# Performance work log

Hardware: AMD Instinct MI355X
Metric: run time of the kernel (lower is better)

Reference implementation:

```python
import jax, jax.numpy as jnp
import numpy as np

# static config (matches init_kwargs)
T_K = 3      # Time_kernel
K = 3        # spatial_kernel_side_length
C = 64       # dim_hidden
H = 4        # num_head
D = 16       # dim_head
NL = 2       # num_layers
F = 3        # dim_feature
N, S1, S2 = 32, 32, 32
P = K // 2
L1 = T_K // 2
M = T_K * K * K
EPS = 1e-5


def _neighbor_mask():
    # spatial_neighbor_mask with an all-ones city mask: offset (k1,k2) is a valid
    # neighbor of cell (s1,s2) iff it lands inside the grid.
    m = np.zeros((S1, S2, K, K), dtype=bool)
    s1 = np.arange(S1); s2 = np.arange(S2)
    for k1 in range(K):
        v1 = (s1 + k1 - P >= 0) & (s1 + k1 - P < S1)
        for k2 in range(K):
            v2 = (s2 + k2 - P >= 0) & (s2 + k2 - P < S2)
            m[:, :, k1, k2] = v1[:, None] & v2[None, :]
    mf = m.reshape(S1, S2, K * K)
    # tiled across Time_kernel, flattened in (t, k1, k2) order like the torch code
    return np.tile(mf[:, :, None, :], (1, 1, T_K, 1)).reshape(S1, S2, M)

_MASK = jnp.asarray(_neighbor_mask())


def _forward(x, W_in, b_in, W_out, b_out, Wq, bq, Wk, bk, Wv, bv):
    # BatchNorm2d (training-mode batch stats, affine = identity init)
    mean = x.mean(axis=(0, 1, 2))
    var = ((x - mean) ** 2).mean(axis=(0, 1, 2))
    h = (x - mean) * jax.lax.rsqrt(var + EPS)
    h = h @ W_in + b_in  # [N,S1,S2,C]

    for l in range(NL):
        res = h  # res_block_thickness = 1 -> residual every layer
        q = (h @ Wq[l] + bq[l]).reshape(N, S1, S2, H, D)
        # spatial unfold (nn.Unfold, padding=K//2, stride=1)
        hp = jnp.pad(h, ((0, 0), (P, P), (P, P), (0, 0)))
        u = jnp.stack([jnp.stack([hp[:, k1:k1 + S1, k2:k2 + S2, :]
                                  for k2 in range(K)]) for k1 in range(K)])  # [K,K,N,S1,S2,C]
        # time unfold (zero-padded shifts along N)
        up = jnp.pad(u, ((0, 0), (0, 0), (L1, L1), (0, 0), (0, 0), (0, 0)))
        ut = jnp.stack([up[:, :, t:t + N] for t in range(T_K)])  # [T,K,K,N,S1,S2,C]
        # per-offset single-Linear MLPs (kernel_neurons=[C,C]), batched over T,K,K
        ks = jnp.einsum('tijnabc,tijcd->nabtijd', ut, Wk[l]) + bk[l]
        vs = jnp.einsum('tijnabc,tijcd->nabtijd', ut, Wv[l]) + bv[l]
        kM = ks.reshape(N, S1, S2, M, H, D)
        vM = vs.reshape(N, S1, S2, M, H, D)
        # unscaled dot-product attention over valid neighbors (masked == dropped)
        sc = jnp.einsum('nabmhd,nabhd->nabhm', kM, q)
        sc = jnp.where(_MASK[None, :, :, None, :], sc, -1e30)
        w = jax.nn.softmax(sc, axis=-1)
        h = jnp.einsum('nabhm,nabmhd->nabhd', w, vM).reshape(N, S1, S2, C)
        h = h + res

    return h @ W_out + b_out  # [N,S1,S2,F]


def setup_inputs() -> dict:
    key = jax.random.key(0)
    k = jax.random.split(key, 11)
    s = 0.05
    return {
        'x': jax.random.normal(k[0], (N, S1, S2, F), jnp.float32),
        'W_in': jax.random.normal(k[1], (F, C), jnp.float32) * s,
        'b_in': jax.random.normal(k[2], (C,), jnp.float32) * s,
        'W_out': jax.random.normal(k[3], (C, F), jnp.float32) * s,
        'b_out': jax.random.normal(k[4], (F,), jnp.float32) * s,
        'Wq': jax.random.normal(k[5], (NL, C, C), jnp.float32) * s,
        'bq': jax.random.normal(k[6], (NL, C), jnp.float32) * s,
        'Wk': jax.random.normal(k[7], (NL, T_K, K, K, C, C), jnp.float32) * s,
        'bk': jax.random.normal(k[8], (NL, T_K, K, K, C), jnp.float32) * s,
        'Wv': jax.random.normal(k[9], (NL, T_K, K, K, C, C), jnp.float32) * s,
        'bv': jax.random.normal(k[10], (NL, T_K, K, K, C), jnp.float32) * s,
    }


def reference(x, W_in, b_in, W_out, b_out, Wq, bq, Wk, bk, Wv, bv):
    return _forward(x, W_in, b_in, W_out, b_out, Wq, bq, Wk, bk, Wv, bv)
```

## Files before the change

### kernel.cpp

```cpp
#include <hip/hip_runtime.h>
#include <hip/hip_bf16.h>


typedef short short8_t __attribute__((ext_vector_type(8)));
typedef float floatx16 __attribute__((ext_vector_type(16)));

__device__ __forceinline__ short f2bs(float f) {
    __hip_bfloat16 h = __float2bfloat16(f);
    return *reinterpret_cast<short*>(&h);
}
__device__ __forceinline__ float bs2f(short s) {
    union { unsigned u; float f; } v;
    v.u = ((unsigned)(unsigned short)s) << 16;
    return v.f;
}
__device__ __forceinline__ int hn_idx(int rowid, int chunk) {
    return rowid * 64 + ((chunk ^ (rowid & 7)) << 3);
}
__device__ __forceinline__ float half_sum(float p) {
    float a = p, b = p;
    asm("v_permlane32_swap_b32 %0, %1" : "+v"(a), "+v"(b));
    return a + b;
}

__global__ void prep_kernel(const float* __restrict__ Wq, const float* __restrict__ Wk,
                            const float* __restrict__ Wv, short* __restrict__ dst,
                            const float* __restrict__ x, float* __restrict__ sums) {
    if (blockIdx.x < 220) {
        int t = blockIdx.x * 256 + threadIdx.x;
        if (t >= 110 * 512) return;
        int mat  = t >> 9;
        int rem  = t & 511;
        int hp   = rem >> 8;
        int kk   = (rem >> 6) & 3;
        int lane = rem & 63;
        int krow = kk * 16 + ((lane >> 5) << 3);
        int col  = hp * 32 + (lane & 31);
        const float* W;
        if (mat < 2)       W = Wq + mat * 4096;
        else if (mat < 56) W = Wk + (mat - 2) * 4096;
        else               W = Wv + (mat - 56) * 4096;
        short8_t v;
        #pragma unroll
        for (int j = 0; j < 8; ++j) v[j] = f2bs(W[(krow + j) * 64 + col]);
        *(short8_t*)&dst[(size_t)mat * 4096 + ((hp * 4 + kk) * 64 + lane) * 8] = v;
    } else {
        int bid = blockIdx.x - 220;
        int t = bid * 256 + threadIdx.x;
        const float4* x4 = (const float4*)x;
        float4 v0 = x4[t * 3 + 0], v1 = x4[t * 3 + 1], v2 = x4[t * 3 + 2];
        float vv[6];
        vv[0] = v0.x + v0.w + v1.z + v2.y;
        vv[1] = v0.y + v1.x + v1.w + v2.z;
        vv[2] = v0.z + v1.y + v2.x + v2.w;
        vv[3] = v0.x*v0.x + v0.w*v0.w + v1.z*v1.z + v2.y*v2.y;
        vv[4] = v0.y*v0.y + v1.x*v1.x + v1.w*v1.w + v2.z*v2.z;
        vv[5] = v0.z*v0.z + v1.y*v1.y + v2.x*v2.x + v2.w*v2.w;
        #pragma unroll
        for (int i = 0; i < 6; ++i) {
            #pragma unroll
            for (int off = 1; off < 64; off <<= 1) vv[i] += __shfl_xor(vv[i], off);
        }
        __shared__ float part[4][6];
        if ((threadIdx.x & 63) == 0) {
            #pragma unroll
            for (int i = 0; i < 6; ++i) part[threadIdx.x >> 6][i] = vv[i];
        }
        __syncthreads();
        if (threadIdx.x < 6)
            sums[bid * 8 + threadIdx.x] = part[0][threadIdx.x] + part[1][threadIdx.x] +
                                          part[2][threadIdx.x] + part[3][threadIdx.x];
    }
}

template <bool FIRST>
__global__ __launch_bounds__(512, 2)
void layer_fused(const float* __restrict__ x, const float* __restrict__ sums,
                 const float* __restrict__ W_in, const float* __restrict__ b_in,
                 const short* __restrict__ hbf_in, short* __restrict__ hbf_out,
                 const float* __restrict__ Wout, const float* __restrict__ bout,
                 float* __restrict__ out,
                 const short* __restrict__ wqB, const float* __restrict__ bq,
                 const short* __restrict__ wkB, const float* __restrict__ bk,
                 const short* __restrict__ wvB, const float* __restrict__ bv) {
    __shared__ short HnS[216 * 64];
    __shared__ float Waux[256];
    __shared__ float bn6[6];

    const int tid = threadIdx.x;
    const int bb0 = blockIdx.x * 2, a = blockIdx.y, nb = blockIdx.z;

    if (FIRST) {
        if (tid < 3) {
            float s = 0.f, qq = 0.f;
            #pragma unroll
            for (int p = 0; p < 32; ++p) { s += sums[p * 8 + tid]; qq += sums[p * 8 + 3 + tid]; }
            float mean = s * (1.f / 32768.f);
            float var  = qq * (1.f / 32768.f) - mean * mean;
            bn6[tid]     = mean;
            bn6[3 + tid] = rsqrtf(var + 1e-5f);
        }
        if (tid < 192)      Waux[tid] = W_in[tid];
        else if (tid < 256) Waux[tid] = b_in[tid - 192];
    } else {
        if (tid < 192)      Waux[tid] = Wout[tid];
        else if (tid < 195) Waux[tid] = bout[tid - 192];
    }
    __syncthreads();

    float mean0 = 0, mean1 = 0, mean2 = 0, rs0 = 0, rs1 = 0, rs2 = 0;
    if (FIRST) {
        mean0 = bn6[0]; mean1 = bn6[1]; mean2 = bn6[2];
        rs0 = bn6[3]; rs1 = bn6[4]; rs2 = bn6[5];
    }

    for (int id = tid; id < 1728; id += 512) {
        int rowid = id >> 3, cc = id & 7;
        int r = rowid % 18;
        int rw = rowid / 18;
        int spa = rw >> 2, jcol = rw & 3;
        int aa = a + spa - 1, bb = bb0 + jcol - 1;
        int n  = nb * 16 + r - 1;
        short8_t v = {0, 0, 0, 0, 0, 0, 0, 0};
        if ((unsigned)n < 32u && (unsigned)aa < 32u && (unsigned)bb < 32u) {
            int cell = (n * 32 + aa) * 32 + bb;
            if (FIRST) {
                float xn0 = (x[cell*3+0] - mean0) * rs0;
                float xn1 = (x[cell*3+1] - mean1) * rs1;
                float xn2 = (x[cell*3+2] - mean2) * rs2;
                #pragma unroll
                for (int j = 0; j < 8; ++j) {
                    int c = cc * 8 + j;
                    float h = Waux[192+c] + xn0*Waux[c] + xn1*Waux[64+c] + xn2*Waux[128+c];
                    v[j] = f2bs(h);
                }
            } else {
                v = *(const short8_t*)&hbf_in[cell * 64 + cc * 8];
            }
        }
        *(short8_t*)&HnS[hn_idx(rowid, cc)] = v;
    }
    __syncthreads();

    const int lane = tid & 63;
    const int wv8  = tid >> 6;
    const int hp   = wv8 & 1;
    const int g4   = wv8 >> 1;
    const int col  = lane & 31;
    const int e    = col & 15;
    const int ci   = col >> 4;
    const int h5   = lane >> 5;

    unsigned amask = 0;
    #pragma unroll
    for (int d = 0; d < 3; ++d) if ((unsigned)(a + d - 1) < 32u) amask |= 1u << d;
    const bool vbL = (unsigned)(bb0 - 1) < 32u;
    const bool vbR = (unsigned)(bb0 + 2) < 32u;
    const unsigned vmask = (ci == 0) ? ((vbL ? 1u : 0u) | 2u | 4u)
                                     : (1u | 2u | (vbR ? 4u : 0u));

    const int elane = e + ci * 18;

    floatx16 qv;
    {
        const float* bqp = &bq[hp * 32 + 4 * h5];
        const float4 qa = *(const float4*)&bqp[0];
        const float4 qb = *(const float4*)&bqp[8];
        const float4 qc = *(const float4*)&bqp[16];
        const float4 qd = *(const float4*)&bqp[24];
        qv = floatx16{qa.x,qa.y,qa.z,qa.w, qb.x,qb.y,qb.z,qb.w,
                      qc.x,qc.y,qc.z,qc.w, qd.x,qd.y,qd.z,qd.w};
        const int hrow = (5 + ci) * 18 + e + 1;
        const int hb = hrow * 64, xr = hrow & 7;
        const short8_t b0 = *(const short8_t*)&HnS[hb + (((0 + h5) ^ xr) << 3)];
        const short8_t b1 = *(const short8_t*)&HnS[hb + (((2 + h5) ^ xr) << 3)];
        const short8_t b2 = *(const short8_t*)&HnS[hb + (((4 + h5) ^ xr) << 3)];
        const short8_t b3 = *(const short8_t*)&HnS[hb + (((6 + h5) ^ xr) << 3)];
        const short8_t* wqp = (const short8_t*)&wqB[(hp * 256 + lane) * 8];
        qv = __builtin_amdgcn_mfma_f32_32x32x16_bf16(wqp[0],   b0, qv, 0, 0, 0);
        qv = __builtin_amdgcn_mfma_f32_32x32x16_bf16(wqp[64],  b1, qv, 0, 0, 0);
        qv = __builtin_amdgcn_mfma_f32_32x32x16_bf16(wqp[128], b2, qv, 0, 0, 0);
        qv = __builtin_amdgcn_mfma_f32_32x32x16_bf16(wqp[192], b3, qv, 0, 0, 0);
    }

    floatx16 o = {0,0,0,0, 0,0,0,0, 0,0,0,0, 0,0,0,0};
    float ssA = 0.f, ssB = 0.f;

    const int mstart = g4 * 7;
    const int mend   = (g4 == 3) ? 27 : mstart + 7;
    for (int m = mstart; m < mend; ++m) {
        const int t  = (m * 57) >> 9;
        const int sp = m - 9 * t;
        const int di = (sp * 11) >> 5;
        const int dj = sp - 3 * di;
        if (!((amask >> di) & 1u)) continue;

        const int hrow = (di * 4 + dj) * 18 + t + elane;
        const int hb = hrow * 64, xr = hrow & 7;
        const short8_t b0 = *(const short8_t*)&HnS[hb + (((0 + h5) ^ xr) << 3)];
        const short8_t b1 = *(const short8_t*)&HnS[hb + (((2 + h5) ^ xr) << 3)];
        const short8_t b2 = *(const short8_t*)&HnS[hb + (((4 + h5) ^ xr) << 3)];
        const short8_t b3 = *(const short8_t*)&HnS[hb + (((6 + h5) ^ xr) << 3)];

        const short8_t* wkp = (const short8_t*)&wkB[m * 4096 + (hp * 256 + lane) * 8];
        const float* bkp = &bk[m * 64 + hp * 32 + 4 * h5];
        const float4 ka = *(const float4*)&bkp[0];
        const float4 kb = *(const float4*)&bkp[8];
        const float4 kc = *(const float4*)&bkp[16];
        const float4 kd = *(const float4*)&bkp[24];
        floatx16 kacc = floatx16{ka.x,ka.y,ka.z,ka.w, kb.x,kb.y,kb.z,kb.w,
                                 kc.x,kc.y,kc.z,kc.w, kd.x,kd.y,kd.z,kd.w};
        kacc = __builtin_amdgcn_mfma_f32_32x32x16_bf16(wkp[0],   b0, kacc, 0, 0, 0);
        kacc = __builtin_amdgcn_mfma_f32_32x32x16_bf16(wkp[64],  b1, kacc, 0, 0, 0);
        kacc = __builtin_amdgcn_mfma_f32_32x32x16_bf16(wkp[128], b2, kacc, 0, 0, 0);
        kacc = __builtin_amdgcn_mfma_f32_32x32x16_bf16(wkp[192], b3, kacc, 0, 0, 0);

        const short8_t* wvp = (const short8_t*)&wvB[m * 4096 + (hp * 256 + lane) * 8];
        const float* bvp = &bv[m * 64 + hp * 32 + 4 * h5];
        const float4 va0 = *(const float4*)&bvp[0];
        const float4 va1 = *(const float4*)&bvp[8];
        const float4 va2 = *(const float4*)&bvp[16];
        const float4 va3 = *(const float4*)&bvp[24];
        floatx16 vacc = floatx16{va0.x,va0.y,va0.z,va0.w, va1.x,va1.y,va1.z,va1.w,
                                 va2.x,va2.y,va2.z,va2.w, va3.x,va3.y,va3.z,va3.w};
        vacc = __builtin_amdgcn_mfma_f32_32x32x16_bf16(wvp[0],   b0, vacc, 0, 0, 0);
        vacc = __builtin_amdgcn_mfma_f32_32x32x16_bf16(wvp[64],  b1, vacc, 0, 0, 0);
        vacc = __builtin_amdgcn_mfma_f32_32x32x16_bf16(wvp[128], b2, vacc, 0, 0, 0);
        vacc = __builtin_amdgcn_mfma_f32_32x32x16_bf16(wvp[192], b3, vacc, 0, 0, 0);

        float pA = kacc[0] * qv[0];
        #pragma unroll
        for (int r = 1; r < 8; ++r) pA += kacc[r] * qv[r];
        float pB = kacc[8] * qv[8];
        #pragma unroll
        for (int r = 9; r < 16; ++r) pB += kacc[r] * qv[r];
        pA = half_sum(pA);
        pB = half_sum(pB);
        const float mf = (float)((vmask >> dj) & 1u);
        const float wA = __expf(pA) * mf;
        const float wB = __expf(pB) * mf;
        ssA += wA; ssB += wB;
        #pragma unroll
        for (int r = 0; r < 8; ++r)  o[r] += wA * vacc[r];
        #pragma unroll
        for (int r = 8; r < 16; ++r) o[r] += wB * vacc[r];
    }

    __syncthreads();
    float* stbuf = (float*)HnS;
    if (g4 >= 2) {
        float* d = &stbuf[(((g4 - 2) * 2 + hp) * 64 + lane) * 20];
        *(float4*)&d[0]  = make_float4(o[0],  o[1],  o[2],  o[3]);
        *(float4*)&d[4]  = make_float4(o[4],  o[5],  o[6],  o[7]);
        *(float4*)&d[8]  = make_float4(o[8],  o[9],  o[10], o[11]);
        *(float4*)&d[12] = make_float4(o[12], o[13], o[14], o[15]);
        *(float2*)&d[16] = make_float2(ssA, ssB);
    }
    __syncthreads();
    if (g4 < 2) {
        const float* d = &stbuf[((g4 * 2 + hp) * 64 + lane) * 20];
        const float4 r0 = *(const float4*)&d[0];
        const float4 r1 = *(const float4*)&d[4];
        const float4 r2 = *(const float4*)&d[8];
        const float4 r3 = *(const float4*)&d[12];
        const float2 rs = *(const float2*)&d[16];
        o[0] += r0.x; o[1] += r0.y; o[2]  += r0.z; o[3]  += r0.w;
        o[4] += r1.x; o[5] += r1.y; o[6]  += r1.z; o[7]  += r1.w;
        o[8] += r2.x; o[9] += r2.y; o[10] += r2.z; o[11] += r2.w;
        o[12] += r3.x; o[13] += r3.y; o[14] += r3.z; o[15] += r3.w;
        ssA += rs.x; ssB += rs.y;
    }
    __syncthreads();
    if (g4 == 1) {
        float* d = &stbuf[(hp * 64 + lane) * 20];
        *(float4*)&d[0]  = make_float4(o[0],  o[1],  o[2],  o[3]);
        *(float4*)&d[4]  = make_float4(o[4],  o[5],  o[6],  o[7]);
        *(float4*)&d[8]  = make_float4(o[8],  o[9],  o[10], o[11]);
        *(float4*)&d[12] = make_float4(o[12], o[13], o[14], o[15]);
        *(float2*)&d[16] = make_float2(ssA, ssB);
    }
    __syncthreads();
    if (g4 == 0) {
        const float* d = &stbuf[(hp * 64 + lane) * 20];
        const float4 r0 = *(const float4*)&d[0];
        const float4 r1 = *(const float4*)&d[4];
        const float4 r2 = *(const float4*)&d[8];
        const float4 r3 = *(const float4*)&d[12];
        const float2 rs = *(const float2*)&d[16];
        o[0] += r0.x; o[1] += r0.y; o[2]  += r0.z; o[3]  += r0.w;
        o[4] += r1.x; o[5] += r1.y; o[6]  += r1.z; o[7]  += r1.w;
        o[8] += r2.x; o[9] += r2.y; o[10] += r2.z; o[11] += r2.w;
        o[12] += r3.x; o[13] += r3.y; o[14] += r3.z; o[15] += r3.w;
        ssA += rs.x; ssB += rs.y;
        const float invA = 1.0f / ssA;
        const float invB = 1.0f / ssB;
        #pragma unroll
        for (int r = 0; r < 8; ++r)  o[r] *= invA;
        #pragma unroll
        for (int r = 8; r < 16; ++r) o[r] *= invB;
    }

    const int n = nb * 16 + e;
    if (FIRST) {
        if (g4 == 0) {
            const int cell = (n * 32 + a) * 32 + bb0 + ci;
            const float xn0 = (x[cell*3+0] - mean0) * rs0;
            const float xn1 = (x[cell*3+1] - mean1) * rs1;
            const float xn2 = (x[cell*3+2] - mean2) * rs2;
            #pragma unroll
            for (int g = 0; g < 4; ++g) {
                short4 hb4; short* hbp = (short*)&hb4;
                #pragma unroll
                for (int i = 0; i < 4; ++i) {
                    const int c = hp * 32 + g * 8 + 4 * h5 + i;
                    const float res = Waux[192+c] + xn0*Waux[c] + xn1*Waux[64+c] + xn2*Waux[128+c];
                    hbp[i] = f2bs(o[g * 4 + i] + res);
                }
                *(short4*)&hbf_out[cell * 64 + hp * 32 + g * 8 + 4 * h5] = hb4;
            }
        }
    } else {
        __syncthreads();
        float* hf = (float*)HnS;
        if (g4 == 0) {
            const int cell = (n * 32 + a) * 32 + bb0 + ci;
            #pragma unroll
            for (int g = 0; g < 4; ++g) {
                const short4 hb4 = *(const short4*)&hbf_in[cell * 64 + hp * 32 + g * 8 + 4 * h5];
                float4 tv = make_float4(o[g*4+0] + bs2f(hb4.x), o[g*4+1] + bs2f(hb4.y),
                                        o[g*4+2] + bs2f(hb4.z), o[g*4+3] + bs2f(hb4.w));
                *(float4*)&hf[col * 68 + hp * 32 + g * 8 + 4 * h5] = tv;
            }
        }
        __syncthreads();
        if (tid < 96) {
            int rowglob = tid / 3, f = tid - rowglob * 3;
            int cio = rowglob >> 4, row = rowglob & 15;
            float acc = Waux[192 + f];
            #pragma unroll 8
            for (int cc = 0; cc < 64; ++cc) acc += hf[rowglob * 68 + cc] * Waux[cc * 3 + f];
            int nn = nb * 16 + row;
            out[((nn * 32 + a) * 32 + bb0 + cio) * 3 + f] = acc;
        }
    }
}

extern "C" void kernel_launch(void* const* d_in, const int* in_sizes, int n_in,
                              void* d_out, int out_size, void* d_ws, size_t ws_size,
                              hipStream_t stream) {
    const float* x     = (const float*)d_in[0];
    const float* W_in  = (const float*)d_in[1];
    const float* b_in  = (const float*)d_in[2];
    const float* W_out = (const float*)d_in[3];
    const float* b_out = (const float*)d_in[4];
    const float* Wq    = (const float*)d_in[5];
    const float* bq    = (const float*)d_in[6];
    const float* Wk    = (const float*)d_in[7];
    const float* bk    = (const float*)d_in[8];
    const float* Wv    = (const float*)d_in[9];
    const float* bv    = (const float*)d_in[10];

    float* ws    = (float*)d_ws;
    float* sums  = ws;
    short* h1bf  = (short*)(ws + 256);
    short* wB    = h1bf + 2097152;
    float* out   = (float*)d_out;

    prep_kernel<<<252, 256, 0, stream>>>(Wq, Wk, Wv, wB, x, sums);

    const short* wq0 = wB;                const short* wq1 = wB + 4096;
    const short* wk0 = wB + 2 * 4096;     const short* wk1 = wB + (2 + 27) * 4096;
    const short* wv0 = wB + 56 * 4096;    const short* wv1 = wB + (56 + 27) * 4096;

    dim3 grid(16, 32, 2);
    layer_fused<true><<<grid, 512, 0, stream>>>(
        x, sums, W_in, b_in, nullptr, h1bf, nullptr, nullptr, nullptr,
        wq0, bq, wk0, bk, wv0, bv);
    layer_fused<false><<<grid, 512, 0, stream>>>(
        nullptr, nullptr, nullptr, nullptr, h1bf, nullptr, W_out, b_out, out,
        wq1, bq + 64, wk1, bk + 1728, wv1, bv + 1728);
}
```

Before: 146.1 us.

## Prefetch key weights, stage biases in LDS, raise occupancy hint, parallelize output projection

Double-buffers the key-weight fragments so the next offset's weights are loaded during the current offset's MFMAs. Biases for keys and values are staged once per block in shared memory rather than read from global memory each iteration. The per-offset branch that skipped masked rows is replaced by a multiplicative mask, so border rows now do the full MFMA work. The launch-bounds occupancy hint goes from 2 to 4 blocks, and the final output projection is split across 384 threads with shuffle reductions. The tighter register budget and the extra shared memory could cause spills or limit how many blocks actually fit per CU.

```diff
diff --git a/kernel.cpp b/kernel.cpp
--- a/kernel.cpp
+++ b/kernel.cpp
@@ -74,7 +74,7 @@
 }
 
 template <bool FIRST>
-__global__ __launch_bounds__(512, 2)
+__global__ __launch_bounds__(512, 4)
 void layer_fused(const float* __restrict__ x, const float* __restrict__ sums,
                  const float* __restrict__ W_in, const float* __restrict__ b_in,
                  const short* __restrict__ hbf_in, short* __restrict__ hbf_out,
@@ -84,6 +84,7 @@
                  const short* __restrict__ wkB, const float* __restrict__ bk,
                  const short* __restrict__ wvB, const float* __restrict__ bv) {
     __shared__ short HnS[216 * 64];
+    __shared__ float BiasS[3456];
     __shared__ float Waux[256];
     __shared__ float bn6[6];
 
@@ -112,6 +113,13 @@
     if (FIRST) {
         mean0 = bn6[0]; mean1 = bn6[1]; mean2 = bn6[2];
         rs0 = bn6[3]; rs1 = bn6[4]; rs2 = bn6[5];
+    }
+
+    for (int id = tid; id < 3456; id += 512) {
+        const int half = (id >= 1728) ? 1 : 0;
+        const int j = id - half * 1728;
+        const float* src = half ? &bv[j] : &bk[j];
+        BiasS[((j >> 6) << 7) + (half << 6) + (j & 63)] = *src;
     }
 
     for (int id = tid; id < 1728; id += 512) {
@@ -188,12 +196,21 @@
 
     const int mstart = g4 * 7;
     const int mend   = (g4 == 3) ? 27 : mstart + 7;
-    for (int m = mstart; m < mend; ++m) {
+
+    const short* wkBase = wkB + hp * 2048 + lane * 8;
+    const short* wvBase = wvB + hp * 2048 + lane * 8;
+
+    short8_t wkX[4], wkY[4];
+    #pragma unroll
+    for (int j = 0; j < 4; ++j)
+        wkX[j] = *(const short8_t*)&wkBase[mstart * 4096 + j * 512];
+
+    auto body = [&](short8_t (&wkc)[4], short8_t (&wkn)[4], const int m) {
+        const int mn = (m + 1 < mend) ? (m + 1) : m;
         const int t  = (m * 57) >> 9;
         const int sp = m - 9 * t;
         const int di = (sp * 11) >> 5;
         const int dj = sp - 3 * di;
-        if (!((amask >> di) & 1u)) continue;
 
         const int hrow = (di * 4 + dj) * 18 + t + elane;
         const int hb = hrow * 64, xr = hrow & 7;
@@ -202,31 +219,38 @@
         const short8_t b2 = *(const short8_t*)&HnS[hb + (((4 + h5) ^ xr) << 3)];
         const short8_t b3 = *(const short8_t*)&HnS[hb + (((6 + h5) ^ xr) << 3)];
 
-        const short8_t* wkp = (const short8_t*)&wkB[m * 4096 + (hp * 256 + lane) * 8];
-        const float* bkp = &bk[m * 64 + hp * 32 + 4 * h5];
-        const float4 ka = *(const float4*)&bkp[0];
-        const float4 kb = *(const float4*)&bkp[8];
-        const float4 kc = *(const float4*)&bkp[16];
-        const float4 kd = *(const float4*)&bkp[24];
+        const float* bks = &BiasS[(m << 7) + (hp << 5) + (h5 << 2)];
+        const float4 ka = *(const float4*)&bks[0];
+        const float4 kb = *(const float4*)&bks[8];
+        const float4 kc = *(const float4*)&bks[16];
+        const float4 kd = *(const float4*)&bks[24];
+        const float4 va0 = *(const float4*)&bks[64];
+        const float4 va1 = *(const float4*)&bks[72];
+        const float4 va2 = *(const float4*)&bks[80];
+        const float4 va3 = *(const float4*)&bks[88];
+
+        const short8_t wv0 = *(const short8_t*)&wvBase[m * 4096 + 0];
+        const short8_t wv1 = *(const short8_t*)&wvBase[m * 4096 + 512];
+        const short8_t wv2 = *(const short8_t*)&wvBase[m * 4096 + 1024];
+        const short8_t wv3 = *(const short8_t*)&wvBase[m * 4096 + 1536];
+
+        #pragma unroll
+        for (int j = 0; j < 4; ++j)
+            wkn[j] = *(const short8_t*)&wkBase[mn * 4096 + j * 512];
+
         floatx16 kacc = floatx16{ka.x,ka.y,ka.z,ka.w, kb.x,kb.y,kb.z,kb.w,
                                  kc.x,kc.y,kc.z,kc.w, kd.x,kd.y,kd.z,kd.w};
-        kacc = __builtin_amdgcn_mfma_f32_32x32x16_bf16(wkp[0],   b0, kacc, 0, 0, 0);
-        kacc = __builtin_amdgcn_mfma_f32_32x32x16_bf16(wkp[64],  b1, kacc, 0, 0, 0);
-        kacc = __builtin_amdgcn_mfma_f32_32x32x16_bf16(wkp[128], b2, kacc, 0, 0, 0);
-        kacc = __builtin_amdgcn_mfma_f32_32x32x16_bf16(wkp[192], b3, kacc, 0, 0, 0);
-
-        const short8_t* wvp = (const short8_t*)&wvB[m * 4096 + (hp * 256 + lane) * 8];
-        const float* bvp = &bv[m * 64 + hp * 32 + 4 * h5];
-        const float4 va0 = *(const float4*)&bvp[0];
-        const float4 va1 = *(const float4*)&bvp[8];
-        const float4 va2 = *(const float4*)&bvp[16];
-        const float4 va3 = *(const float4*)&bvp[24];
+        kacc = __builtin_amdgcn_mfma_f32_32x32x16_bf16(wkc[0], b0, kacc, 0, 0, 0);
+        kacc = __builtin_amdgcn_mfma_f32_32x32x16_bf16(wkc[1], b1, kacc, 0, 0, 0);
+        kacc = __builtin_amdgcn_mfma_f32_32x32x16_bf16(wkc[2], b2, kacc, 0, 0, 0);
+        kacc = __builtin_amdgcn_mfma_f32_32x32x16_bf16(wkc[3], b3, kacc, 0, 0, 0);
+
         floatx16 vacc = floatx16{va0.x,va0.y,va0.z,va0.w, va1.x,va1.y,va1.z,va1.w,
                                  va2.x,va2.y,va2.z,va2.w, va3.x,va3.y,va3.z,va3.w};
-        vacc = __builtin_amdgcn_mfma_f32_32x32x16_bf16(wvp[0],   b0, vacc, 0, 0, 0);
-        vacc = __builtin_amdgcn_mfma_f32_32x32x16_bf16(wvp[64],  b1, vacc, 0, 0, 0);
-        vacc = __builtin_amdgcn_mfma_f32_32x32x16_bf16(wvp[128], b2, vacc, 0, 0, 0);
-        vacc = __builtin_amdgcn_mfma_f32_32x32x16_bf16(wvp[192], b3, vacc, 0, 0, 0);
+        vacc = __builtin_amdgcn_mfma_f32_32x32x16_bf16(wv0, b0, vacc, 0, 0, 0);
+        vacc = __builtin_amdgcn_mfma_f32_32x32x16_bf16(wv1, b1, vacc, 0, 0, 0);
+        vacc = __builtin_amdgcn_mfma_f32_32x32x16_bf16(wv2, b2, vacc, 0, 0, 0);
+        vacc = __builtin_amdgcn_mfma_f32_32x32x16_bf16(wv3, b3, vacc, 0, 0, 0);
 
         float pA = kacc[0] * qv[0];
         #pragma unroll
@@ -236,7 +260,7 @@
         for (int r = 9; r < 16; ++r) pB += kacc[r] * qv[r];
         pA = half_sum(pA);
         pB = half_sum(pB);
-        const float mf = (float)((vmask >> dj) & 1u);
+        const float mf = (float)(((amask >> di) & (vmask >> dj)) & 1u);
         const float wA = __expf(pA) * mf;
         const float wB = __expf(pB) * mf;
         ssA += wA; ssB += wB;
@@ -244,6 +268,11 @@
         for (int r = 0; r < 8; ++r)  o[r] += wA * vacc[r];
         #pragma unroll
         for (int r = 8; r < 16; ++r) o[r] += wB * vacc[r];
+    };
+
+    for (int m = mstart; m < mend; m += 2) {
+        body(wkX, wkY, m);
+        if (m + 1 < mend) body(wkY, wkX, m + 1);
     }
 
     __syncthreads();
@@ -333,14 +362,21 @@
             }
         }
         __syncthreads();
-        if (tid < 96) {
-            int rowglob = tid / 3, f = tid - rowglob * 3;
-            int cio = rowglob >> 4, row = rowglob & 15;
-            float acc = Waux[192 + f];
-            #pragma unroll 8
-            for (int cc = 0; cc < 64; ++cc) acc += hf[rowglob * 68 + cc] * Waux[cc * 3 + f];
-            int nn = nb * 16 + row;
-            out[((nn * 32 + a) * 32 + bb0 + cio) * 3 + f] = acc;
+        if (tid < 384) {
+            const int oid = tid >> 2, part = tid & 3;
+            const int rowglob = oid / 3, f = oid - rowglob * 3;
+            const int cstart = part << 4;
+            float acc = 0.f;
+            #pragma unroll
+            for (int cc = 0; cc < 16; ++cc)
+                acc += hf[rowglob * 68 + cstart + cc] * Waux[(cstart + cc) * 3 + f];
+            acc += __shfl_xor(acc, 1);
+            acc += __shfl_xor(acc, 2);
+            if (part == 0) {
+                const int cio = rowglob >> 4, row = rowglob & 15;
+                out[(((nb * 16 + row) * 32 + a) * 32 + bb0 + cio) * 3 + f] =
+                    acc + Waux[192 + f];
+            }
         }
     }
 }
```

Result: no change. 143.4 us (-1.9%).
